# Kernel tuning notes

Hardware: AMD Instinct MI355X
Metric: run time of the kernel (lower is better)

## Reference

```python
import jax, jax.numpy as jnp
import numpy as np

B, N, E = 16, 4096, 65536
IN, H, GOUT = 128, 512, 8
F0, F1, F2 = 3, 64, 64
D1, D2 = 512, 32768  # MLP: H -> D1 -> D2, D2 == N*GOUT
EPS = 1e-5


def _lin_init(k, fan_in, shape):
    bound = 1.0 / np.sqrt(fan_in)
    return jax.random.uniform(k, shape, jnp.float32, -bound, bound)


def setup_inputs() -> dict:
    key = jax.random.key(0)
    ks = jax.random.split(key, 40)
    inp = {}
    inp['x'] = jax.random.normal(ks[0], (B, IN), jnp.float32)
    inp['smoothed_vert_pos'] = jax.random.normal(ks[1], (B, N * 3), jnp.float32)
    inp['hidden'] = jnp.zeros((B, H), jnp.float32)
    inp['edge_index'] = jax.random.randint(ks[2], (2, E), 0, N, dtype=jnp.int32)
    # GCN layers (W stored [in,out])
    inp['W_gcn0'] = _lin_init(ks[3], F0, (F0, F1)); inp['b_gcn0'] = jnp.zeros((F1,), jnp.float32)
    inp['W_gcn1'] = _lin_init(ks[4], F1, (F1, F2)); inp['b_gcn1'] = jnp.zeros((F2,), jnp.float32)
    # GRUCell (torch layout: [3H, in], gate order r,z,n)
    inp['w_ih'] = _lin_init(ks[5], H, (3 * H, IN)); inp['b_ih'] = _lin_init(ks[6], H, (3 * H,))
    inp['w_hh'] = _lin_init(ks[7], H, (3 * H, H)); inp['b_hh'] = _lin_init(ks[8], H, (3 * H,))
    # MLP layer 1: H -> D1 (Linear + PReLU + BatchNorm1d eval)
    inp['mlp_w1'] = _lin_init(ks[9], H, (H, D1)); inp['mlp_b1'] = _lin_init(ks[10], H, (D1,))
    inp['alpha1'] = 0.25 * jnp.ones((D1,), jnp.float32)
    inp['bn1_gamma'] = jnp.ones((D1,), jnp.float32); inp['bn1_beta'] = jnp.zeros((D1,), jnp.float32)
    inp['bn1_mean'] = 0.01 * jax.random.normal(ks[11], (D1,), jnp.float32)
    inp['bn1_var'] = jnp.ones((D1,), jnp.float32)
    # MLP layer 2: D1 -> D2
    inp['mlp_w2'] = _lin_init(ks[12], D1, (D1, D2)); inp['mlp_b2'] = _lin_init(ks[13], D1, (D2,))
    inp['alpha2'] = 0.25 * jnp.ones((D2,), jnp.float32)
    inp['bn2_gamma'] = jnp.ones((D2,), jnp.float32); inp['bn2_beta'] = jnp.zeros((D2,), jnp.float32)
    inp['bn2_mean'] = 0.01 * jax.random.normal(ks[14], (D2,), jnp.float32)
    inp['bn2_var'] = jnp.ones((D2,), jnp.float32)
    # output head: (F2 + GOUT) -> 3
    inp['w_out'] = _lin_init(ks[15], F2 + GOUT, (F2 + GOUT, 3)); inp['b_out'] = _lin_init(ks[16], F2 + GOUT, (3,))
    return inp


def _forward(edge_index, x, smoothed_vert_pos, hidden,
             W_gcn0, b_gcn0, W_gcn1, b_gcn1,
             w_ih, w_hh, b_ih, b_hh,
             mlp_w1, mlp_b1, alpha1, bn1_gamma, bn1_beta, bn1_mean, bn1_var,
             mlp_w2, mlp_b2, alpha2, bn2_gamma, bn2_beta, bn2_mean, bn2_var,
             w_out, b_out):
    Bb = x.shape[0]
    pos = smoothed_vert_pos.reshape(Bb, N, 3)
    # GCN normalization with added self-loops (PyG gcn_norm, eval: no edge dropout)
    loop = jnp.arange(N, dtype=edge_index.dtype)
    src = jnp.concatenate([edge_index[0], loop])
    dst = jnp.concatenate([edge_index[1], loop])
    deg = jax.ops.segment_sum(jnp.ones_like(dst, jnp.float32), dst, num_segments=N)
    dis = jnp.where(deg > 0, jax.lax.rsqrt(deg), 0.0)
    norm = dis[src] * dis[dst]  # [E+N]

    def gcn(h, W, b):
        hw = jnp.einsum('bnf,fg->bng', h, W)                       # [B,N,G]
        msg = hw[:, src, :] * norm[None, :, None]                   # [B,E+N,G]
        agg = jax.ops.segment_sum(jnp.swapaxes(msg, 0, 1), dst, num_segments=N)  # [N,B,G]
        return jnp.swapaxes(agg, 0, 1) + b

    h0 = gcn(pos, W_gcn0, b_gcn0)
    h1 = gcn(h0, W_gcn1, b_gcn1)
    h1 = jax.lax.stop_gradient(h1)  # eval-mode .detach()

    # GRUCell (torch gate order r,z,n)
    gi = x @ w_ih.T + b_ih
    gh = hidden @ w_hh.T + b_hh
    ir, iz, inn = jnp.split(gi, 3, axis=1)
    hr, hz, hn = jnp.split(gh, 3, axis=1)
    r = jax.nn.sigmoid(ir + hr)
    z = jax.nn.sigmoid(iz + hz)
    n = jnp.tanh(inn + r * hn)
    next_hidden = (1.0 - z) * n + z * hidden

    def mlp_block(v, w, b, alpha, g, bt, mean, var):
        v = v @ w + b
        v = jnp.where(v > 0, v, alpha * v)                          # PReLU
        return g * (v - mean) * jax.lax.rsqrt(var + EPS) + bt       # BN eval

    m = mlp_block(next_hidden, mlp_w1, mlp_b1, alpha1, bn1_gamma, bn1_beta, bn1_mean, bn1_var)
    m = mlp_block(m, mlp_w2, mlp_b2, alpha2, bn2_gamma, bn2_beta, bn2_mean, bn2_var)
    gru_out = m.reshape(Bb, N, GOUT)
    y = jnp.concatenate([gru_out, h1], axis=2) @ w_out + b_out      # [B,N,3]
    return y.reshape(Bb, -1), next_hidden


def reference(x, smoothed_vert_pos, hidden, edge_index,
              W_gcn0, b_gcn0, W_gcn1, b_gcn1,
              w_ih, b_ih, w_hh, b_hh,
              mlp_w1, mlp_b1, alpha1, bn1_gamma, bn1_beta, bn1_mean, bn1_var,
              mlp_w2, mlp_b2, alpha2, bn2_gamma, bn2_beta, bn2_mean, bn2_var,
              w_out, b_out):
    return _forward(edge_index, x, smoothed_vert_pos, hidden,
                    W_gcn0, b_gcn0, W_gcn1, b_gcn1,
                    w_ih, w_hh, b_ih, b_hh,
                    mlp_w1, mlp_b1, alpha1, bn1_gamma, bn1_beta, bn1_mean, bn1_var,
                    mlp_w2, mlp_b2, alpha2, bn2_gamma, bn2_beta, bn2_mean, bn2_var,
                    w_out, b_out)
```

## Files before the change

kernel.cpp:

```cpp
#include <hip/hip_runtime.h>
#include <math.h>

#define BB 16
#define NN 4096
#define EE 65536
#define IN_F 128
#define HH 512
#define D1 512
#define D2 32768
#define EPSV 1e-5f
#define CAP 64


__global__ __launch_bounds__(256) void k_stageA(
        int* __restrict__ csr2, int* __restrict__ cursor,
        const float* __restrict__ W0, const float* __restrict__ b0,
        const float* __restrict__ W1, const float* __restrict__ b1,
        const float* __restrict__ w_out, float* __restrict__ sm,
        const float* __restrict__ x, const float* __restrict__ hidden,
        const float* __restrict__ w_ih, const float* __restrict__ b_ih,
        const float* __restrict__ w_hh, const float* __restrict__ b_hh,
        float* __restrict__ nh_out, float* __restrict__ nh_ws) {
    __shared__ float s_x[16 * 128];
    __shared__ float s_h[16 * 512];
    __shared__ float s_p[6 * 256];
    int bid = blockIdx.x;
    int tid = threadIdx.x;
    if (bid < 1024) {
        csr2[bid * 256 + tid] = NN;
        return;
    }
    if (bid < 1040) {
        cursor[(bid - 1024) * 256 + tid] = 0;
        return;
    }
    if (bid == 1040) {
        float* sm3 = s_p;
        if (tid < 192) {
            int f = tid / 3, c = tid - 3 * (tid / 3);
            float acc = 0.f;
            for (int g = 0; g < 64; ++g) acc += W1[f * 64 + g] * w_out[(8 + g) * 3 + c];
            sm3[tid] = acc;
        }
        __syncthreads();
        if (tid < 9) {
            int k = tid / 3, c = tid - 3 * (tid / 3);
            float acc = 0.f;
            for (int f = 0; f < 64; ++f) acc += W0[k * 64 + f] * sm3[f * 3 + c];
            sm[tid] = acc;
        } else if (tid < 12) {
            int c = tid - 9;
            float acc = 0.f;
            for (int f = 0; f < 64; ++f) acc += b0[f] * sm3[f * 3 + c];
            sm[tid] = acc;
        } else if (tid < 15) {
            int c = tid - 12;
            float acc = 0.f;
            for (int g = 0; g < 64; ++g) acc += b1[g] * w_out[(8 + g) * 3 + c];
            sm[tid] = acc;
        }
        return;
    }
    int jb = bid - 1041;
    int j0 = jb * 4;
    for (int i = tid; i < 512; i += 256) ((float4*)s_x)[i] = ((const float4*)x)[i];
    for (int i = tid; i < 2048; i += 256) ((float4*)s_h)[i] = ((const float4*)hidden)[i];
    __syncthreads();
    int b = tid & 15, jl = (tid >> 4) & 3, q = tid >> 6;
    int j = j0 + jl;
    float air = 0.f, aiz = 0.f, ain = 0.f, ahr = 0.f, ahz = 0.f, ahn = 0.f;
    {
        const float4* xi = (const float4*)(s_x + b * 128 + q * 32);
        const float4* w0 = (const float4*)(w_ih + (size_t)j * IN_F + q * 32);
        const float4* w1 = (const float4*)(w_ih + (size_t)(HH + j) * IN_F + q * 32);
        const float4* w2 = (const float4*)(w_ih + (size_t)(2 * HH + j) * IN_F + q * 32);
#pragma unroll
        for (int i = 0; i < 8; ++i) {
            float4 xv = xi[i];
            float4 a = w0[i], c = w1[i], d = w2[i];
            air += xv.x * a.x + xv.y * a.y + xv.z * a.z + xv.w * a.w;
            aiz += xv.x * c.x + xv.y * c.y + xv.z * c.z + xv.w * c.w;
            ain += xv.x * d.x + xv.y * d.y + xv.z * d.z + xv.w * d.w;
        }
    }
    {
        const float4* hi = (const float4*)(s_h + b * 512 + q * 128);
        const float4* w0 = (const float4*)(w_hh + (size_t)j * HH + q * 128);
        const float4* w1 = (const float4*)(w_hh + (size_t)(HH + j) * HH + q * 128);
        const float4* w2 = (const float4*)(w_hh + (size_t)(2 * HH + j) * HH + q * 128);
#pragma unroll 8
        for (int i = 0; i < 32; ++i) {
            float4 hv = hi[i];
            float4 a = w0[i], c = w1[i], d = w2[i];
            ahr += hv.x * a.x + hv.y * a.y + hv.z * a.z + hv.w * a.w;
            ahz += hv.x * c.x + hv.y * c.y + hv.z * c.z + hv.w * c.w;
            ahn += hv.x * d.x + hv.y * d.y + hv.z * d.z + hv.w * d.w;
        }
    }
    int pi = q * 64 + jl * 16 + b;
    s_p[0 * 256 + pi] = air; s_p[1 * 256 + pi] = aiz; s_p[2 * 256 + pi] = ain;
    s_p[3 * 256 + pi] = ahr; s_p[4 * 256 + pi] = ahz; s_p[5 * 256 + pi] = ahn;
    __syncthreads();
    if (tid < 64) {
        int b2 = tid & 15, jl2 = tid >> 4;
        int jj = j0 + jl2;
        float v0 = 0.f, v1 = 0.f, v2 = 0.f, v3 = 0.f, v4 = 0.f, v5 = 0.f;
#pragma unroll
        for (int qq = 0; qq < 4; ++qq) {
            int idx = qq * 64 + jl2 * 16 + b2;
            v0 += s_p[0 * 256 + idx]; v1 += s_p[1 * 256 + idx]; v2 += s_p[2 * 256 + idx];
            v3 += s_p[3 * 256 + idx]; v4 += s_p[4 * 256 + idx]; v5 += s_p[5 * 256 + idx];
        }
        float ir = v0 + b_ih[jj], iz = v1 + b_ih[HH + jj], inn = v2 + b_ih[2 * HH + jj];
        float hr = v3 + b_hh[jj], hz = v4 + b_hh[HH + jj], hn = v5 + b_hh[2 * HH + jj];
        float r = 1.f / (1.f + expf(-(ir + hr)));
        float z = 1.f / (1.f + expf(-(iz + hz)));
        float nn = tanhf(inn + r * hn);
        float hprev = s_h[b2 * 512 + jj];
        float nh = (1.f - z) * nn + z * hprev;
        nh_out[b2 * HH + jj] = nh;
        nh_ws[b2 * HH + jj] = nh;
    }
}


__global__ void k_stageB(const int* __restrict__ src, const int* __restrict__ dst,
                         int* __restrict__ cursor, int* __restrict__ csr2,
                         const float* __restrict__ nh, const float* __restrict__ w1,
                         const float* __restrict__ b1v, const float* __restrict__ alpha1,
                         const float* __restrict__ g1, const float* __restrict__ bt1,
                         const float* __restrict__ mu1, const float* __restrict__ var1,
                         float* __restrict__ m1) {
    __shared__ float s_nh[512];
    __shared__ float s_p[4 * 64];
    int bid = blockIdx.x;
    int tid = threadIdx.x;
    if (bid < 256) {
        int i = bid * 256 + tid;
        int d = dst[i];
        int slot = atomicAdd(&cursor[d], 1);
        if (slot < CAP) csr2[d * CAP + slot] = src[i];
        return;
    }
    int mb = bid - 256;
    int b = mb >> 3;
    int jblk = mb & 7;
    for (int i = tid; i < 512; i += 256) s_nh[i] = nh[b * HH + i];
    __syncthreads();
    int jloc = tid & 63;
    int ks = tid >> 6;
    int j = jblk * 64 + jloc;
    const float* wp = w1 + (size_t)(ks * 128) * D1 + j;
    float acc = 0.f;
#pragma unroll 4
    for (int k0 = 0; k0 < 128; k0 += 4) {
        float w0 = wp[0], w1v = wp[D1], w2v = wp[2 * D1], w3v = wp[3 * D1];
        float4 mv = *(const float4*)&s_nh[ks * 128 + k0];
        acc += mv.x * w0 + mv.y * w1v + mv.z * w2v + mv.w * w3v;
        wp += 4 * D1;
    }
    s_p[ks * 64 + jloc] = acc;
    __syncthreads();
    if (tid < 64) {
        int jj = jblk * 64 + tid;
        float v = s_p[tid] + s_p[64 + tid] + s_p[128 + tid] + s_p[192 + tid];
        v += b1v[jj];
        float al = alpha1[jj];
        v = v > 0.f ? v : al * v;
        float iv = rsqrtf(var1[jj] + EPSV);
        m1[b * D1 + jj] = g1[jj] * (v - mu1[jj]) * iv + bt1[jj];
    }
}


__device__ __forceinline__ void mlp2_unit(int jt, int ok, const float* __restrict__ m1,
                                          const float* __restrict__ w2,
                                          float* __restrict__ part,
                                          float* s_m1, int tid) {
    {
        int b = tid >> 4, kg = tid & 15;
        *(float4*)&s_m1[b * 64 + kg * 4] = *(const float4*)(m1 + b * 512 + ok * 64 + kg * 4);
    }
    __syncthreads();
    int j = jt * 512 + tid * 2;
    const float* wp = w2 + (size_t)(ok * 64) * D2 + j;
    float2 wb0 = *(const float2*)(wp + 0 * (size_t)D2);
    float2 wb1 = *(const float2*)(wp + 1 * (size_t)D2);
    float2 wb2 = *(const float2*)(wp + 2 * (size_t)D2);
    float2 wb3 = *(const float2*)(wp + 3 * (size_t)D2);
    float acc0[16], acc1[16];
#pragma unroll
    for (int b = 0; b < 16; ++b) { acc0[b] = 0.f; acc1[b] = 0.f; }
    for (int k4 = 0; k4 < 64; k4 += 4) {
        float2 c0 = wb0, c1 = wb1, c2 = wb2, c3 = wb3;
        int kp = (k4 + 4 < 64) ? k4 + 4 : 0;
        wb0 = *(const float2*)(wp + (size_t)(kp + 0) * D2);
        wb1 = *(const float2*)(wp + (size_t)(kp + 1) * D2);
        wb2 = *(const float2*)(wp + (size_t)(kp + 2) * D2);
        wb3 = *(const float2*)(wp + (size_t)(kp + 3) * D2);
#pragma unroll
        for (int b = 0; b < 16; ++b) {
            float2 p01 = *(const float2*)&s_m1[b * 64 + k4];
            float2 p23 = *(const float2*)&s_m1[b * 64 + k4 + 2];
            acc0[b] += p01.x * c0.x + p01.y * c1.x + p23.x * c2.x + p23.y * c3.x;
            acc1[b] += p01.x * c0.y + p01.y * c1.y + p23.x * c2.y + p23.y * c3.y;
        }
    }
    float* pb = part + (size_t)(ok * 16) * D2 + j;
#pragma unroll
    for (int b = 0; b < 16; ++b) {
        *(float2*)(pb + (size_t)b * D2) = make_float2(acc0[b], acc1[b]);
    }
}


__global__ void k_stageC(const int* __restrict__ cursor,
                         const float* __restrict__ pos, float* __restrict__ v0,
                         const float* __restrict__ m1, const float* __restrict__ w2,
                         float* __restrict__ part) {
    __shared__ float smem[1024];
    int bid = blockIdx.x;
    int tid = threadIdx.x;
    if (bid < 512) {
        mlp2_unit(bid >> 3, bid & 7, m1, w2, part, smem, tid);
        return;
    }
    int vb = bid - 512;
    int n = vb * 4 + (tid >> 6);
    int l = tid & 63;
    if (n > NN) return;
    if (n == NN) { v0[(size_t)NN * 64 + l] = 0.f; return; }
    int b = l >> 2, c = l & 3;
    float val = 0.f;
    if (c < 3) {
        float d = rsqrtf((float)(cursor[n] + 1));
        val = d * pos[(size_t)b * (NN * 3) + n * 3 + c];
    }
    v0[(size_t)n * 64 + l] = val;
}


__global__ __launch_bounds__(256) void k_stageD(
        const float* __restrict__ v0, const int* __restrict__ cursor,
        const int* __restrict__ csr2, const float* __restrict__ sm,
        float* __restrict__ u) {
    __shared__ int sidx[4][CAP];
    __shared__ float sP[4][64];
    int tid = threadIdx.x;
    int w = tid >> 6;
    int l = tid & 63;
    int n = blockIdx.x * 4 + w;
    if (n > NN) return;
    if (n == NN) { u[(size_t)NN * 64 + l] = 0.f; return; }
    const int* row = csr2 + n * CAP;
    sidx[w][l] = row[l];
    int deg = cursor[n];
    if (deg > CAP) deg = CAP;
    float acc = v0[(size_t)n * 64 + l];
    int nch = (deg + 7) >> 3;
    float A[8], B[8];
    if (nch > 0) {
#pragma unroll
        for (int i = 0; i < 8; ++i) A[i] = v0[(size_t)sidx[w][i] * 64 + l];
    }
    for (int c = 0; c < nch; ++c) {
        if (c + 1 < nch) {
            int base = (c + 1) * 8;
#pragma unroll
            for (int i = 0; i < 8; ++i) B[i] = v0[(size_t)sidx[w][base + i] * 64 + l];
        }
#pragma unroll
        for (int i = 0; i < 8; ++i) acc += A[i];
        if (c + 1 < nch) {
#pragma unroll
            for (int i = 0; i < 8; ++i) A[i] = B[i];
        }
    }
    sP[w][l] = acc;
    int base = l & ~3;
    float P0 = sP[w][base + 0], P1 = sP[w][base + 1], P2 = sP[w][base + 2];
    int c = l & 3;
    float d = rsqrtf((float)(cursor[n] + 1));
    float uu = 0.f;
    if (c < 3)
        uu = d * d * (P0 * sm[c] + P1 * sm[3 + c] + P2 * sm[6 + c]) + d * sm[9 + c];
    u[(size_t)n * 64 + l] = uu;
}


__global__ __launch_bounds__(256) void k_stageE(
        const float* __restrict__ u, const int* __restrict__ cursor,
        const int* __restrict__ csr2, const float* __restrict__ sm,
        const float* __restrict__ part,
        const float* __restrict__ b2, const float* __restrict__ alpha2,
        const float* __restrict__ g2, const float* __restrict__ bt2,
        const float* __restrict__ mu2, const float* __restrict__ var2,
        const float* __restrict__ w_out, const float* __restrict__ b_out,
        float* __restrict__ y) {
    __shared__ int sidx[4][CAP];
    __shared__ float sV[4][128];
    int w = threadIdx.x >> 6;
    int l = threadIdx.x & 63;
    int n = blockIdx.x * 4 + w;
    const int* row = csr2 + n * CAP;
    sidx[w][l] = row[l];
    const float4* pr0 = (const float4*)(part + (size_t)l * D2 + n * 8);
    const float4* pr1 = (const float4*)(part + (size_t)(64 + l) * D2 + n * 8);
    float4 ra0 = pr0[0], ra1 = pr0[1];
    float4 rb0 = pr1[0], rb1 = pr1[1];
    int deg = cursor[n];
    if (deg > CAP) deg = CAP;
    float acc = u[(size_t)n * 64 + l];
    int nch = (deg + 7) >> 3;
    float A[8], B[8];
    if (nch > 0) {
#pragma unroll
        for (int i = 0; i < 8; ++i) A[i] = u[(size_t)sidx[w][i] * 64 + l];
    }
    for (int c = 0; c < nch; ++c) {
        if (c + 1 < nch) {
            int base = (c + 1) * 8;
#pragma unroll
            for (int i = 0; i < 8; ++i) B[i] = u[(size_t)sidx[w][base + i] * 64 + l];
        }
#pragma unroll
        for (int i = 0; i < 8; ++i) acc += A[i];
        if (c + 1 < nch) {
#pragma unroll
            for (int i = 0; i < 8; ++i) A[i] = B[i];
        }
    }
    float d = rsqrtf((float)(cursor[n] + 1));
    float hval = d * acc + (((l & 3) < 3) ? sm[12 + (l & 3)] : 0.f);
    float vg[8] = {ra0.x + rb0.x, ra0.y + rb0.y, ra0.z + rb0.z, ra0.w + rb0.w,
                   ra1.x + rb1.x, ra1.y + rb1.y, ra1.z + rb1.z, ra1.w + rb1.w};
#pragma unroll
    for (int g = 0; g < 8; ++g) vg[g] += __shfl_xor(vg[g], 16);
#pragma unroll
    for (int g = 0; g < 8; ++g) vg[g] += __shfl_xor(vg[g], 32);
    if (l < 16) {
#pragma unroll
        for (int g = 0; g < 8; ++g) {
            int j = n * 8 + g;
            float v = vg[g] + b2[j];
            float al = alpha2[j];
            v = v > 0.f ? v : al * v;
            v = g2[j] * (v - mu2[j]) * rsqrtf(var2[j] + EPSV) + bt2[j];
            sV[w][g * 16 + l] = v;
        }
    }
    __syncthreads();
    int bb = l >> 2, c = l & 3;
    if (c < 3) {
        float y0 = b_out[c] + hval;
#pragma unroll
        for (int g = 0; g < 8; ++g) y0 += sV[w][g * 16 + bb] * w_out[g * 3 + c];
        y[(size_t)bb * (NN * 3) + n * 3 + c] = y0;
    }
}


extern "C" void kernel_launch(void* const* d_in, const int* in_sizes, int n_in,
                              void* d_out, int out_size, void* d_ws, size_t ws_size,
                              hipStream_t stream) {
    const float* x      = (const float*)d_in[0];
    const float* pos    = (const float*)d_in[1];
    const float* hidden = (const float*)d_in[2];
    const int*   ei     = (const int*)d_in[3];
    const float* W0     = (const float*)d_in[4];
    const float* b0     = (const float*)d_in[5];
    const float* W1     = (const float*)d_in[6];
    const float* b1     = (const float*)d_in[7];
    const float* w_ih   = (const float*)d_in[8];
    const float* b_ih   = (const float*)d_in[9];
    const float* w_hh   = (const float*)d_in[10];
    const float* b_hh   = (const float*)d_in[11];
    const float* mlp_w1 = (const float*)d_in[12];
    const float* mlp_b1 = (const float*)d_in[13];
    const float* alpha1 = (const float*)d_in[14];
    const float* bn1g   = (const float*)d_in[15];
    const float* bn1b   = (const float*)d_in[16];
    const float* bn1m   = (const float*)d_in[17];
    const float* bn1v   = (const float*)d_in[18];
    const float* mlp_w2 = (const float*)d_in[19];
    const float* mlp_b2 = (const float*)d_in[20];
    const float* alpha2 = (const float*)d_in[21];
    const float* bn2g   = (const float*)d_in[22];
    const float* bn2b   = (const float*)d_in[23];
    const float* bn2m   = (const float*)d_in[24];
    const float* bn2v   = (const float*)d_in[25];
    const float* w_out  = (const float*)d_in[26];
    const float* b_out  = (const float*)d_in[27];

    float* out = (float*)d_out;
    float* ws = (float*)d_ws;

    float* v0   = ws;
    float* u    = ws + 262208;
    float* part = ws + 524416;
    float* nh   = ws + 4718720;
    float* m1   = ws + 4726912;
    float* sm   = ws + 4735104;
    int* wsi    = (int*)(ws + 4735120);
    int* cursor = wsi;
    int* csr2   = wsi + 4096;

    const int* srcp = ei;
    const int* dstp = ei + EE;

    k_stageA<<<1024 + 16 + 1 + 128, 256, 0, stream>>>(csr2, cursor, W0, b0, W1, b1, w_out,
                                                      sm, x, hidden, w_ih, b_ih, w_hh,
                                                      b_hh, out + BB * NN * 3, nh);
    k_stageB<<<256 + 128, 256, 0, stream>>>(srcp, dstp, cursor, csr2, nh, mlp_w1, mlp_b1,
                                            alpha1, bn1g, bn1b, bn1m, bn1v, m1);
    k_stageC<<<512 + 1025, 256, 0, stream>>>(cursor, pos, v0, m1, mlp_w2, part);
    k_stageD<<<1025, 256, 0, stream>>>(v0, cursor, csr2, sm, u);
    k_stageE<<<1024, 256, 0, stream>>>(u, cursor, csr2, sm, part, mlp_b2, alpha2, bn2g,
                                       bn2b, bn2m, bn2v, w_out, b_out, out);
}
```

Baseline: 58.11 us.

## Fuse first GCN aggregation into MLP2 stage and drop a kernel launch

The degree-independent position transpose moves into stage A, so the first neighbor aggregation can run inside the MLP2 kernel with per-neighbor degree normalization applied on the fly. This removes one kernel launch and one grid-wide dependency. The GRU blocks are also moved to the front of stage A so they get scheduled first. The cost is an extra cursor load and rsqrt per gathered neighbor, and the cursor region is padded to 4352 ints (17 blocks zeroed), so cursor[NN] is now zero for the padding node.

Measured after the change: 51.64 us (median of 2 runs). 1.13x faster.

```diff
diff --git a/kernel.cpp b/kernel.cpp
--- a/kernel.cpp
+++ b/kernel.cpp
@@ -17,6 +17,7 @@
         const float* __restrict__ W0, const float* __restrict__ b0,
         const float* __restrict__ W1, const float* __restrict__ b1,
         const float* __restrict__ w_out, float* __restrict__ sm,
+        const float* __restrict__ pos, float* __restrict__ pv,
         const float* __restrict__ x, const float* __restrict__ hidden,
         const float* __restrict__ w_ih, const float* __restrict__ b_ih,
         const float* __restrict__ w_hh, const float* __restrict__ b_hh,
@@ -26,15 +27,78 @@
     __shared__ float s_p[6 * 256];
     int bid = blockIdx.x;
     int tid = threadIdx.x;
-    if (bid < 1024) {
-        csr2[bid * 256 + tid] = NN;
-        return;
-    }
-    if (bid < 1040) {
-        cursor[(bid - 1024) * 256 + tid] = 0;
-        return;
-    }
-    if (bid == 1040) {
+    if (bid < 128) {
+        int jb = bid;
+        int j0 = jb * 4;
+        for (int i = tid; i < 512; i += 256) ((float4*)s_x)[i] = ((const float4*)x)[i];
+        for (int i = tid; i < 2048; i += 256) ((float4*)s_h)[i] = ((const float4*)hidden)[i];
+        __syncthreads();
+        int b = tid & 15, jl = (tid >> 4) & 3, q = tid >> 6;
+        int j = j0 + jl;
+        float air = 0.f, aiz = 0.f, ain = 0.f, ahr = 0.f, ahz = 0.f, ahn = 0.f;
+        {
+            const float4* xi = (const float4*)(s_x + b * 128 + q * 32);
+            const float4* w0 = (const float4*)(w_ih + (size_t)j * IN_F + q * 32);
+            const float4* w1 = (const float4*)(w_ih + (size_t)(HH + j) * IN_F + q * 32);
+            const float4* w2 = (const float4*)(w_ih + (size_t)(2 * HH + j) * IN_F + q * 32);
+#pragma unroll
+            for (int i = 0; i < 8; ++i) {
+                float4 xv = xi[i];
+                float4 a = w0[i], c = w1[i], d = w2[i];
+                air += xv.x * a.x + xv.y * a.y + xv.z * a.z + xv.w * a.w;
+                aiz += xv.x * c.x + xv.y * c.y + xv.z * c.z + xv.w * c.w;
+                ain += xv.x * d.x + xv.y * d.y + xv.z * d.z + xv.w * d.w;
+            }
+        }
+        {
+            const float4* hi = (const float4*)(s_h + b * 512 + q * 128);
+            const float4* w0 = (const float4*)(w_hh + (size_t)j * HH + q * 128);
+            const float4* w1 = (const float4*)(w_hh + (size_t)(HH + j) * HH + q * 128);
+            const float4* w2 = (const float4*)(w_hh + (size_t)(2 * HH + j) * HH + q * 128);
+#pragma unroll 8
+            for (int i = 0; i < 32; ++i) {
+                float4 hv = hi[i];
+                float4 a = w0[i], c = w1[i], d = w2[i];
+                ahr += hv.x * a.x + hv.y * a.y + hv.z * a.z + hv.w * a.w;
+                ahz += hv.x * c.x + hv.y * c.y + hv.z * c.z + hv.w * c.w;
+                ahn += hv.x * d.x + hv.y * d.y + hv.z * d.z + hv.w * d.w;
+            }
+        }
+        int pi = q * 64 + jl * 16 + b;
+        s_p[0 * 256 + pi] = air; s_p[1 * 256 + pi] = aiz; s_p[2 * 256 + pi] = ain;
+        s_p[3 * 256 + pi] = ahr; s_p[4 * 256 + pi] = ahz; s_p[5 * 256 + pi] = ahn;
+        __syncthreads();
+        if (tid < 64) {
+            int b2 = tid & 15, jl2 = tid >> 4;
+            int jj = j0 + jl2;
+            float v0 = 0.f, v1 = 0.f, v2 = 0.f, v3 = 0.f, v4 = 0.f, v5 = 0.f;
+#pragma unroll
+            for (int qq = 0; qq < 4; ++qq) {
+                int idx = qq * 64 + jl2 * 16 + b2;
+                v0 += s_p[0 * 256 + idx]; v1 += s_p[1 * 256 + idx]; v2 += s_p[2 * 256 + idx];
+                v3 += s_p[3 * 256 + idx]; v4 += s_p[4 * 256 + idx]; v5 += s_p[5 * 256 + idx];
+            }
+            float ir = v0 + b_ih[jj], iz = v1 + b_ih[HH + jj], inn = v2 + b_ih[2 * HH + jj];
+            float hr = v3 + b_hh[jj], hz = v4 + b_hh[HH + jj], hn = v5 + b_hh[2 * HH + jj];
+            float r = 1.f / (1.f + expf(-(ir + hr)));
+            float z = 1.f / (1.f + expf(-(iz + hz)));
+            float nn = tanhf(inn + r * hn);
+            float hprev = s_h[b2 * 512 + jj];
+            float nh = (1.f - z) * nn + z * hprev;
+            nh_out[b2 * HH + jj] = nh;
+            nh_ws[b2 * HH + jj] = nh;
+        }
+        return;
+    }
+    if (bid < 1152) {
+        csr2[(bid - 128) * 256 + tid] = NN;
+        return;
+    }
+    if (bid < 1169) {
+        cursor[(bid - 1152) * 256 + tid] = 0;
+        return;
+    }
+    if (bid == 1169) {
         float* sm3 = s_p;
         if (tid < 192) {
             int f = tid / 3, c = tid - 3 * (tid / 3);
@@ -61,66 +125,14 @@
         }
         return;
     }
-    int jb = bid - 1041;
-    int j0 = jb * 4;
-    for (int i = tid; i < 512; i += 256) ((float4*)s_x)[i] = ((const float4*)x)[i];
-    for (int i = tid; i < 2048; i += 256) ((float4*)s_h)[i] = ((const float4*)hidden)[i];
-    __syncthreads();
-    int b = tid & 15, jl = (tid >> 4) & 3, q = tid >> 6;
-    int j = j0 + jl;
-    float air = 0.f, aiz = 0.f, ain = 0.f, ahr = 0.f, ahz = 0.f, ahn = 0.f;
-    {
-        const float4* xi = (const float4*)(s_x + b * 128 + q * 32);
-        const float4* w0 = (const float4*)(w_ih + (size_t)j * IN_F + q * 32);
-        const float4* w1 = (const float4*)(w_ih + (size_t)(HH + j) * IN_F + q * 32);
-        const float4* w2 = (const float4*)(w_ih + (size_t)(2 * HH + j) * IN_F + q * 32);
-#pragma unroll
-        for (int i = 0; i < 8; ++i) {
-            float4 xv = xi[i];
-            float4 a = w0[i], c = w1[i], d = w2[i];
-            air += xv.x * a.x + xv.y * a.y + xv.z * a.z + xv.w * a.w;
-            aiz += xv.x * c.x + xv.y * c.y + xv.z * c.z + xv.w * c.w;
-            ain += xv.x * d.x + xv.y * d.y + xv.z * d.z + xv.w * d.w;
-        }
-    }
-    {
-        const float4* hi = (const float4*)(s_h + b * 512 + q * 128);
-        const float4* w0 = (const float4*)(w_hh + (size_t)j * HH + q * 128);
-        const float4* w1 = (const float4*)(w_hh + (size_t)(HH + j) * HH + q * 128);
-        const float4* w2 = (const float4*)(w_hh + (size_t)(2 * HH + j) * HH + q * 128);
-#pragma unroll 8
-        for (int i = 0; i < 32; ++i) {
-            float4 hv = hi[i];
-            float4 a = w0[i], c = w1[i], d = w2[i];
-            ahr += hv.x * a.x + hv.y * a.y + hv.z * a.z + hv.w * a.w;
-            ahz += hv.x * c.x + hv.y * c.y + hv.z * c.z + hv.w * c.w;
-            ahn += hv.x * d.x + hv.y * d.y + hv.z * d.z + hv.w * d.w;
-        }
-    }
-    int pi = q * 64 + jl * 16 + b;
-    s_p[0 * 256 + pi] = air; s_p[1 * 256 + pi] = aiz; s_p[2 * 256 + pi] = ain;
-    s_p[3 * 256 + pi] = ahr; s_p[4 * 256 + pi] = ahz; s_p[5 * 256 + pi] = ahn;
-    __syncthreads();
-    if (tid < 64) {
-        int b2 = tid & 15, jl2 = tid >> 4;
-        int jj = j0 + jl2;
-        float v0 = 0.f, v1 = 0.f, v2 = 0.f, v3 = 0.f, v4 = 0.f, v5 = 0.f;
-#pragma unroll
-        for (int qq = 0; qq < 4; ++qq) {
-            int idx = qq * 64 + jl2 * 16 + b2;
-            v0 += s_p[0 * 256 + idx]; v1 += s_p[1 * 256 + idx]; v2 += s_p[2 * 256 + idx];
-            v3 += s_p[3 * 256 + idx]; v4 += s_p[4 * 256 + idx]; v5 += s_p[5 * 256 + idx];
-        }
-        float ir = v0 + b_ih[jj], iz = v1 + b_ih[HH + jj], inn = v2 + b_ih[2 * HH + jj];
-        float hr = v3 + b_hh[jj], hz = v4 + b_hh[HH + jj], hn = v5 + b_hh[2 * HH + jj];
-        float r = 1.f / (1.f + expf(-(ir + hr)));
-        float z = 1.f / (1.f + expf(-(iz + hz)));
-        float nn = tanhf(inn + r * hn);
-        float hprev = s_h[b2 * 512 + jj];
-        float nh = (1.f - z) * nn + z * hprev;
-        nh_out[b2 * HH + jj] = nh;
-        nh_ws[b2 * HH + jj] = nh;
-    }
+    int vb = bid - 1170;
+    int n = vb * 4 + (tid >> 6);
+    int l = tid & 63;
+    if (n > NN) return;
+    if (n == NN) { pv[(size_t)NN * 64 + l] = 0.f; return; }
+    int b = l >> 2, c = l & 3;
+    float val = (c < 3) ? pos[(size_t)b * (NN * 3) + n * 3 + c] : 0.f;
+    pv[(size_t)n * 64 + l] = val;
 }
 
 
@@ -214,81 +226,71 @@
 }
 
 
-__global__ void k_stageC(const int* __restrict__ cursor,
-                         const float* __restrict__ pos, float* __restrict__ v0,
-                         const float* __restrict__ m1, const float* __restrict__ w2,
-                         float* __restrict__ part) {
+__global__ __launch_bounds__(256) void k_stageC(
+        const float* __restrict__ m1, const float* __restrict__ w2,
+        float* __restrict__ part, const float* __restrict__ pv,
+        const int* __restrict__ cursor, const int* __restrict__ csr2,
+        const float* __restrict__ sm, float* __restrict__ u) {
     __shared__ float smem[1024];
+    __shared__ int sidx[4][CAP];
+    __shared__ float sP[4][64];
     int bid = blockIdx.x;
     int tid = threadIdx.x;
     if (bid < 512) {
         mlp2_unit(bid >> 3, bid & 7, m1, w2, part, smem, tid);
         return;
     }
-    int vb = bid - 512;
-    int n = vb * 4 + (tid >> 6);
-    int l = tid & 63;
-    if (n > NN) return;
-    if (n == NN) { v0[(size_t)NN * 64 + l] = 0.f; return; }
-    int b = l >> 2, c = l & 3;
-    float val = 0.f;
-    if (c < 3) {
-        float d = rsqrtf((float)(cursor[n] + 1));
-        val = d * pos[(size_t)b * (NN * 3) + n * 3 + c];
-    }
-    v0[(size_t)n * 64 + l] = val;
-}
-
-
-__global__ __launch_bounds__(256) void k_stageD(
-        const float* __restrict__ v0, const int* __restrict__ cursor,
-        const int* __restrict__ csr2, const float* __restrict__ sm,
-        float* __restrict__ u) {
-    __shared__ int sidx[4][CAP];
-    __shared__ float sP[4][64];
-    int tid = threadIdx.x;
+    int gb = bid - 512;
     int w = tid >> 6;
     int l = tid & 63;
-    int n = blockIdx.x * 4 + w;
+    int n = gb * 4 + w;
     if (n > NN) return;
     if (n == NN) { u[(size_t)NN * 64 + l] = 0.f; return; }
     const int* row = csr2 + n * CAP;
     sidx[w][l] = row[l];
-    int deg = cursor[n];
-    if (deg > CAP) deg = CAP;
-    float acc = v0[(size_t)n * 64 + l];
+    int degc = cursor[n];
+    int deg = degc < CAP ? degc : CAP;
+    float dn = rsqrtf((float)(degc + 1));
+    float acc = dn * pv[(size_t)n * 64 + l];
     int nch = (deg + 7) >> 3;
-    float A[8], B[8];
+    float A[8], B[8], cA[8], cB[8];
     if (nch > 0) {
 #pragma unroll
-        for (int i = 0; i < 8; ++i) A[i] = v0[(size_t)sidx[w][i] * 64 + l];
+        for (int i = 0; i < 8; ++i) {
+            int s = sidx[w][i];
+            A[i] = pv[(size_t)s * 64 + l];
+            cA[i] = (float)cursor[s];
+        }
     }
     for (int c = 0; c < nch; ++c) {
         if (c + 1 < nch) {
             int base = (c + 1) * 8;
 #pragma unroll
-            for (int i = 0; i < 8; ++i) B[i] = v0[(size_t)sidx[w][base + i] * 64 + l];
-        }
-#pragma unroll
-        for (int i = 0; i < 8; ++i) acc += A[i];
+            for (int i = 0; i < 8; ++i) {
+                int s = sidx[w][base + i];
+                B[i] = pv[(size_t)s * 64 + l];
+                cB[i] = (float)cursor[s];
+            }
+        }
+#pragma unroll
+        for (int i = 0; i < 8; ++i) acc += rsqrtf(cA[i] + 1.f) * A[i];
         if (c + 1 < nch) {
 #pragma unroll
-            for (int i = 0; i < 8; ++i) A[i] = B[i];
+            for (int i = 0; i < 8; ++i) { A[i] = B[i]; cA[i] = cB[i]; }
         }
     }
     sP[w][l] = acc;
     int base = l & ~3;
     float P0 = sP[w][base + 0], P1 = sP[w][base + 1], P2 = sP[w][base + 2];
     int c = l & 3;
-    float d = rsqrtf((float)(cursor[n] + 1));
     float uu = 0.f;
     if (c < 3)
-        uu = d * d * (P0 * sm[c] + P1 * sm[3 + c] + P2 * sm[6 + c]) + d * sm[9 + c];
+        uu = dn * dn * (P0 * sm[c] + P1 * sm[3 + c] + P2 * sm[6 + c]) + dn * sm[9 + c];
     u[(size_t)n * 64 + l] = uu;
 }
 
 
-__global__ __launch_bounds__(256) void k_stageE(
+__global__ __launch_bounds__(256) void k_stageD(
         const float* __restrict__ u, const int* __restrict__ cursor,
         const int* __restrict__ csr2, const float* __restrict__ sm,
         const float* __restrict__ part,
@@ -308,8 +310,8 @@
     const float4* pr1 = (const float4*)(part + (size_t)(64 + l) * D2 + n * 8);
     float4 ra0 = pr0[0], ra1 = pr0[1];
     float4 rb0 = pr1[0], rb1 = pr1[1];
-    int deg = cursor[n];
-    if (deg > CAP) deg = CAP;
+    int degc = cursor[n];
+    int deg = degc < CAP ? degc : CAP;
     float acc = u[(size_t)n * 64 + l];
     int nch = (deg + 7) >> 3;
     float A[8], B[8];
@@ -330,7 +332,7 @@
             for (int i = 0; i < 8; ++i) A[i] = B[i];
         }
     }
-    float d = rsqrtf((float)(cursor[n] + 1));
+    float d = rsqrtf((float)(degc + 1));
     float hval = d * acc + (((l & 3) < 3) ? sm[12 + (l & 3)] : 0.f);
     float vg[8] = {ra0.x + rb0.x, ra0.y + rb0.y, ra0.z + rb0.z, ra0.w + rb0.w,
                    ra1.x + rb1.x, ra1.y + rb1.y, ra1.z + rb1.z, ra1.w + rb1.w};
@@ -395,7 +397,7 @@
     float* out = (float*)d_out;
     float* ws = (float*)d_ws;
 
-    float* v0   = ws;
+    float* pv   = ws;
     float* u    = ws + 262208;
     float* part = ws + 524416;
     float* nh   = ws + 4718720;
@@ -403,18 +405,17 @@
     float* sm   = ws + 4735104;
     int* wsi    = (int*)(ws + 4735120);
     int* cursor = wsi;
-    int* csr2   = wsi + 4096;
+    int* csr2   = wsi + 4352;
 
     const int* srcp = ei;
     const int* dstp = ei + EE;
 
-    k_stageA<<<1024 + 16 + 1 + 128, 256, 0, stream>>>(csr2, cursor, W0, b0, W1, b1, w_out,
-                                                      sm, x, hidden, w_ih, b_ih, w_hh,
-                                                      b_hh, out + BB * NN * 3, nh);
+    k_stageA<<<128 + 1024 + 17 + 1 + 1025, 256, 0, stream>>>(
+        csr2, cursor, W0, b0, W1, b1, w_out, sm, pos, pv, x, hidden, w_ih, b_ih, w_hh,
+        b_hh, out + BB * NN * 3, nh);
     k_stageB<<<256 + 128, 256, 0, stream>>>(srcp, dstp, cursor, csr2, nh, mlp_w1, mlp_b1,
                                             alpha1, bn1g, bn1b, bn1m, bn1v, m1);
-    k_stageC<<<512 + 1025, 256, 0, stream>>>(cursor, pos, v0, m1, mlp_w2, part);
-    k_stageD<<<1025, 256, 0, stream>>>(v0, cursor, csr2, sm, u);
-    k_stageE<<<1024, 256, 0, stream>>>(u, cursor, csr2, sm, part, mlp_b2, alpha2, bn2g,
+    k_stageC<<<512 + 1025, 256, 0, stream>>>(m1, mlp_w2, part, pv, cursor, csr2, sm, u);
+    k_stageD<<<1024, 256, 0, stream>>>(u, cursor, csr2, sm, part, mlp_b2, alpha2, bn2g,
                                        bn2b, bn2m, bn2v, w_out, b_out, out);
 }
```
